# Performance work log

Measured on AMD Instinct MI355X. Metric: run time of the kernel, lower is better.

The kernel has to match this reference:

```python
import jax, jax.numpy as jnp
import numpy as np

B, A, C, G = 16, 65472, 81, 50
POS_THRESH = 0.5        # positive_threshold
NEG_POS_RATIO = 3
CENTER_VAR, SIZE_VAR = 0.1, 0.2   # standard SSD encoding variances
BETA = 1.0 / 9


def _make_boxes(key, shape):
    # random valid corner-form boxes in [0,1]
    k1, k2 = jax.random.split(key)
    cxy = jax.random.uniform(k1, shape + (2,), minval=0.1, maxval=0.9)
    wh = jax.random.uniform(k2, shape + (2,), minval=0.05, maxval=0.3)
    lo = jnp.clip(cxy - wh / 2, 0.0, 1.0)
    hi = jnp.clip(cxy + wh / 2, 0.0, 1.0)
    return jnp.concatenate([lo, hi], axis=-1).astype(jnp.float32)


def setup_inputs() -> dict:
    key = jax.random.key(0)
    ks = jax.random.split(key, 6)
    confidence = jax.random.normal(ks[0], (B, A, C), dtype=jnp.float32)
    predicted_locations = jax.random.normal(ks[1], (B, A, 4), dtype=jnp.float32)
    boxes = _make_boxes(ks[2], (B, G))
    labels = jax.random.randint(ks[3], (B, G, 1), 1, C).astype(jnp.float32)
    gts = jnp.concatenate([boxes, labels], axis=-1)          # (B, G, 5)
    counts = jax.random.randint(ks[4], (B,), 1, G + 1)       # valid gt per image
    anchors = _make_boxes(ks[5], (A,))                        # corner form
    return {"confidence": confidence, "predicted_locations": predicted_locations,
            "gts": gts, "counts": counts, "anchors": anchors}


def _center_form(b):
    # corner (x1,y1,x2,y2) -> center (cx,cy,w,h)
    return jnp.concatenate([(b[..., :2] + b[..., 2:]) * 0.5,
                            b[..., 2:] - b[..., :2]], axis=-1)


def _iou(a, b):
    # a: (A,4), b: (G,4), corner form -> (A,G)
    lt = jnp.maximum(a[:, None, :2], b[None, :, :2])
    rb = jnp.minimum(a[:, None, 2:], b[None, :, 2:])
    wh = jnp.clip(rb - lt, 0.0)
    inter = wh[..., 0] * wh[..., 1]
    area_a = (a[:, 2] - a[:, 0]) * (a[:, 3] - a[:, 1])
    area_b = (b[:, 2] - b[:, 0]) * (b[:, 3] - b[:, 1])
    return inter / (area_a[:, None] + area_b[None, :] - inter + 1e-10)


def _encode(matched, anchors_c):
    m = _center_form(matched)
    g_cxcy = (m[..., :2] - anchors_c[..., :2]) / (anchors_c[..., 2:] * CENTER_VAR)
    g_wh = jnp.log(m[..., 2:] / anchors_c[..., 2:] + 1e-10) / SIZE_VAR
    return jnp.concatenate([g_cxcy, g_wh], axis=-1)


def _match(gt, count, anchors, anchors_c):
    # gt: (G,5), count: scalar int
    boxes = gt[:, :4]
    glabels = gt[:, 4].astype(jnp.int32)
    valid = jnp.arange(boxes.shape[0]) < count
    ious = jnp.where(valid[None, :], _iou(anchors, boxes), -1.0)  # (A,G)
    best_iou = ious.max(axis=1)          # best gt per anchor
    best_idx = ious.argmax(axis=1)
    best_anchor = ious.argmax(axis=0)    # best anchor per gt (G,)
    # force-match: each valid gt claims its best anchor (invalid -> dropped)
    scat = jnp.where(valid, best_anchor, anchors.shape[0])
    best_idx = best_idx.at[scat].set(jnp.arange(boxes.shape[0]), mode='drop')
    best_iou = best_iou.at[scat].set(2.0, mode='drop')
    labels = jnp.where(best_iou < POS_THRESH, 0, glabels[best_idx])  # (A,)
    loc = _encode(boxes[best_idx], anchors_c)                         # (A,4)
    return labels, loc


def reference(confidence, predicted_locations, gts, counts, anchors):
    anchors_c = _center_form(anchors)
    labels, gt_locations = jax.vmap(
        lambda g, c: _match(g, c, anchors, anchors_c))(gts, counts)
    labels = jax.lax.stop_gradient(labels)
    gt_locations = jax.lax.stop_gradient(gt_locations)

    logp = jax.nn.log_softmax(confidence, axis=2)          # (B,A,C)
    pos_mask = labels > 0
    num_pos_b = pos_mask.sum(axis=1)                        # (B,)

    # hard negative mining on background loss (positives excluded via -inf)
    mining = jnp.where(pos_mask, -jnp.inf, jax.lax.stop_gradient(-logp[:, :, 0]))
    order = jnp.argsort(-mining, axis=1)   # descending
    rank = jnp.argsort(order, axis=1)
    neg_mask = rank < (NEG_POS_RATIO * num_pos_b)[:, None]
    mask = pos_mask | neg_mask

    num_pos = jnp.maximum(1.0, pos_mask.sum().astype(jnp.float32))

    # masked cross-entropy (sum) == F.cross_entropy(conf[mask], labels[mask], 'sum')
    ce = -jnp.take_along_axis(logp, labels[..., None], axis=2)[..., 0]
    classification_loss = jnp.sum(jnp.where(mask, ce, 0.0)) / (num_pos * 4.0)

    # smooth L1 over positive anchors only
    n = jnp.abs(predicted_locations - gt_locations)
    sl1 = jnp.where(n < BETA, 0.5 * n * n / BETA, n - 0.5 * BETA)
    localisation_loss = jnp.sum(jnp.where(pos_mask[..., None], sl1, 0.0)) / (num_pos * 4.0)
    return (localisation_loss, classification_loss)
```

## Files before the change

### kernel.cpp

```cpp
#include <hip/hip_runtime.h>
#include <math.h>

#define Bn 16
#define An 65472
#define Cn 81
#define Gn 50
#define ROWS 64
#define NCH 8
#define CHUNK_F4 1296
#define LD_T 216
#define LD_K 6
#define NCHH 4
#define NBUCK 1024
#define LISTCAP 8192

static_assert((Bn * (long long)An) % (ROWS * NCH) == 0, "grid covers rows exactly");
static_assert(LD_T * LD_K == CHUNK_F4, "uniform load split");
static_assert((An / 4) % NCHH == 0, "hist chunks divide");

constexpr float POS_THRESH_C = 0.5f;
constexpr float BETA_C = 1.0f / 9.0f;

typedef const __attribute__((address_space(1))) void GPTR;
typedef __attribute__((address_space(3))) void LPTR;

__global__ __launch_bounds__(256) void k1a(const float* __restrict__ anchors,
                                           const float* __restrict__ gts,
                                           const int* __restrict__ counts,
                                           float* __restrict__ best_iou,
                                           int* __restrict__ best_idx,
                                           int* __restrict__ numpos_b,
                                           float* __restrict__ fsums) {
    const int b = blockIdx.y;
    __shared__ float sg[Gn * 5];
    const int t = threadIdx.x;
    if (blockIdx.x == 0 && b == 0) {
        if (t < Bn) numpos_b[t] = 0;
        if (t == Bn) { fsums[0] = 0.f; fsums[1] = 0.f; }
    }
    if (t < Gn * 5) sg[t] = gts[b * Gn * 5 + t];
    __syncthreads();
    const int a = blockIdx.x * 256 + t;
    if (a >= An) return;
    const int cnt = counts[b];
    const float4 av = ((const float4*)anchors)[a];
    const float area_a = (av.z - av.x) * (av.w - av.y);
    float best = -1.0f;
    int bidx = 0;
    for (int g = 0; g < Gn; ++g) {
        if (g >= cnt) break;
        const float bx0 = sg[g * 5 + 0], by0 = sg[g * 5 + 1];
        const float bx1 = sg[g * 5 + 2], by1 = sg[g * 5 + 3];
        const float w = fmaxf(fminf(av.z, bx1) - fmaxf(av.x, bx0), 0.f);
        const float h = fmaxf(fminf(av.w, by1) - fmaxf(av.y, by0), 0.f);
        const float inter = w * h;
        const float area_b = (bx1 - bx0) * (by1 - by0);
        const float iou = inter / (area_a + area_b - inter + 1e-10f);
        if (iou > best) { best = iou; bidx = g; }
    }
    best_iou[(size_t)b * An + a] = best;
    best_idx[(size_t)b * An + a] = bidx;
}

__global__ __launch_bounds__(256) void k1b(const float* __restrict__ anchors,
                                           const float* __restrict__ gts,
                                           const int* __restrict__ counts,
                                           int* __restrict__ best_anchor) {
    const int b = blockIdx.y, g = blockIdx.x;
    const int t = threadIdx.x;
    const int cnt = counts[b];
    if (g >= cnt) { if (t == 0) best_anchor[b * Gn + g] = 0; return; }
    const float bx0 = gts[(b * Gn + g) * 5 + 0], by0 = gts[(b * Gn + g) * 5 + 1];
    const float bx1 = gts[(b * Gn + g) * 5 + 2], by1 = gts[(b * Gn + g) * 5 + 3];
    const float area_b = (bx1 - bx0) * (by1 - by0);
    const float4* a4 = (const float4*)anchors;
    float best = -2.f;
    int bidx = 0x7fffffff;
    for (int base = t; base < An; base += 1024) {
        const int a1 = base + 256, a2 = base + 512, a3 = base + 768;
        const float4 av0 = a4[base];
        float4 av1, av2, av3;
        const bool ok1 = a1 < An, ok2 = a2 < An, ok3 = a3 < An;
        if (ok1) av1 = a4[a1];
        if (ok2) av2 = a4[a2];
        if (ok3) av3 = a4[a3];
        {
            const float area_a = (av0.z - av0.x) * (av0.w - av0.y);
            const float w = fmaxf(fminf(av0.z, bx1) - fmaxf(av0.x, bx0), 0.f);
            const float h = fmaxf(fminf(av0.w, by1) - fmaxf(av0.y, by0), 0.f);
            const float inter = w * h;
            const float iou = inter / (area_a + area_b - inter + 1e-10f);
            if (iou > best) { best = iou; bidx = base; }
        }
        if (ok1) {
            const float area_a = (av1.z - av1.x) * (av1.w - av1.y);
            const float w = fmaxf(fminf(av1.z, bx1) - fmaxf(av1.x, bx0), 0.f);
            const float h = fmaxf(fminf(av1.w, by1) - fmaxf(av1.y, by0), 0.f);
            const float inter = w * h;
            const float iou = inter / (area_a + area_b - inter + 1e-10f);
            if (iou > best) { best = iou; bidx = a1; }
        }
        if (ok2) {
            const float area_a = (av2.z - av2.x) * (av2.w - av2.y);
            const float w = fmaxf(fminf(av2.z, bx1) - fmaxf(av2.x, bx0), 0.f);
            const float h = fmaxf(fminf(av2.w, by1) - fmaxf(av2.y, by0), 0.f);
            const float inter = w * h;
            const float iou = inter / (area_a + area_b - inter + 1e-10f);
            if (iou > best) { best = iou; bidx = a2; }
        }
        if (ok3) {
            const float area_a = (av3.z - av3.x) * (av3.w - av3.y);
            const float w = fmaxf(fminf(av3.z, bx1) - fmaxf(av3.x, bx0), 0.f);
            const float h = fmaxf(fminf(av3.w, by1) - fmaxf(av3.y, by0), 0.f);
            const float inter = w * h;
            const float iou = inter / (area_a + area_b - inter + 1e-10f);
            if (iou > best) { best = iou; bidx = a3; }
        }
    }
    __shared__ float rv[256];
    __shared__ int ri[256];
    rv[t] = best; ri[t] = bidx;
    __syncthreads();
    for (int s = 128; s > 0; s >>= 1) {
        if (t < s) {
            const float fv = rv[t + s]; const int fi = ri[t + s];
            if (fv > rv[t] || (fv == rv[t] && fi < ri[t])) { rv[t] = fv; ri[t] = fi; }
        }
        __syncthreads();
    }
    if (t == 0) best_anchor[b * Gn + g] = ri[0];
}

__global__ __launch_bounds__(64) void k1c(const int* __restrict__ counts,
                                          const int* __restrict__ best_anchor,
                                          float* __restrict__ best_iou,
                                          int* __restrict__ best_idx) {
    const int b = threadIdx.x;
    if (b >= Bn) return;
    const int cnt = counts[b] < Gn ? counts[b] : Gn;
    for (int g = 0; g < cnt; ++g) {
        const int a = best_anchor[b * Gn + g];
        best_idx[(size_t)b * An + a] = g;
        best_iou[(size_t)b * An + a] = 2.0f;
    }
}

__global__ __launch_bounds__(256) void k2(const float* __restrict__ conf,
                                          const float* __restrict__ pred,
                                          const float* __restrict__ gts,
                                          const float* __restrict__ anchors,
                                          const float* __restrict__ best_iou,
                                          const int* __restrict__ best_idx,
                                          int* __restrict__ v_int,
                                          int* __restrict__ numpos_b,
                                          float* __restrict__ fsums) {
    __shared__ __align__(16) float sc[2][ROWS * Cn];
    __shared__ float s_ce[4], s_loc[4];
    __shared__ int s_n0[4], s_n1[4];
    const int t = threadIdx.x;
    const size_t rowbase = (size_t)blockIdx.x * (ROWS * NCH);
    const float* gbase = conf + rowbase * Cn;

    if (t < LD_T) {
#pragma unroll
        for (int k = 0; k < LD_K; ++k) {
            const int c = k * LD_T + t;
            __builtin_amdgcn_global_load_lds((GPTR*)(gbase + c * 4), (LPTR*)(&sc[0][0] + c * 4), 16, 0, 0);
        }
    }

    const int bf = (int)(rowbase / An);
    const int r = t >> 2, h = t & 3;
    const int j0 = h * 20 + (h != 0);
    const int j1 = 21 + h * 20;
    float ce = 0.f, loc = 0.f;
    int n0 = 0, n1 = 0;

    for (int cc = 0; cc < NCH; ++cc) {
        if (cc + 1 < NCH) {
            if (t < LD_T) {
                const float* gp = gbase + (size_t)(cc + 1) * (ROWS * Cn);
                float* lp = &sc[(cc + 1) & 1][0];
#pragma unroll
                for (int k = 0; k < LD_K; ++k) {
                    const int c = k * LD_T + t;
                    __builtin_amdgcn_global_load_lds((GPTR*)(gp + c * 4), (LPTR*)(lp + c * 4), 16, 0, 0);
                }
            }
            asm volatile("s_waitcnt vmcnt(6)" ::: "memory");
        } else {
            asm volatile("s_waitcnt vmcnt(0)" ::: "memory");
        }
        __builtin_amdgcn_sched_barrier(0);
        __builtin_amdgcn_s_barrier();
        asm volatile("" ::: "memory");

        const float* row = &sc[cc & 1][0] + r * Cn;
        float s0 = 0.f, s1 = 0.f;
        for (int j = j0; j + 1 < j1; j += 2) { s0 += __expf(row[j]); s1 += __expf(row[j + 1]); }
        if (((j1 - j0) & 1) != 0) s0 += __expf(row[j1 - 1]);
        float s = s0 + s1;
        s += __shfl_xor(s, 1);
        s += __shfl_xor(s, 2);
        const float lse = logf(s);

        if (h == 0) {
            const size_t gidx = rowbase + (size_t)cc * ROWS + r;
            const int b = (int)(gidx / An);
            const int a = (int)(gidx - (size_t)b * An);
            const float bi = best_iou[gidx];
            const int idx = best_idx[gidx];
            if (bi < POS_THRESH_C) {
                v_int[gidx] = __float_as_int(lse - row[0]);
            } else {
                v_int[gidx] = -1;
                int lab = (int)gts[((size_t)b * Gn + idx) * 5 + 4];
                lab = lab < 0 ? 0 : (lab > Cn - 1 ? Cn - 1 : lab);
                ce += lse - row[lab];
                if (b == bf) ++n0; else ++n1;
                const float bx0 = gts[((size_t)b * Gn + idx) * 5 + 0];
                const float by0 = gts[((size_t)b * Gn + idx) * 5 + 1];
                const float bx1 = gts[((size_t)b * Gn + idx) * 5 + 2];
                const float by1 = gts[((size_t)b * Gn + idx) * 5 + 3];
                const float4 av = ((const float4*)anchors)[a];
                const float acx = (av.x + av.z) * 0.5f, acy = (av.y + av.w) * 0.5f;
                const float aw = av.z - av.x, ah = av.w - av.y;
                float tt[4];
                tt[0] = ((bx0 + bx1) * 0.5f - acx) / (aw * 0.1f);
                tt[1] = ((by0 + by1) * 0.5f - acy) / (ah * 0.1f);
                tt[2] = logf((bx1 - bx0) / aw + 1e-10f) / 0.2f;
                tt[3] = logf((by1 - by0) / ah + 1e-10f) / 0.2f;
                const float4 p = ((const float4*)pred)[gidx];
                const float pk[4] = {p.x, p.y, p.z, p.w};
#pragma unroll
                for (int k = 0; k < 4; ++k) {
                    const float nn = fabsf(pk[k] - tt[k]);
                    loc += (nn < BETA_C) ? 0.5f * nn * nn / BETA_C : nn - 0.5f * BETA_C;
                }
            }
        }
        asm volatile("" ::: "memory");
        __builtin_amdgcn_s_barrier();
    }

#pragma unroll
    for (int off = 32; off > 0; off >>= 1) {
        ce += __shfl_down(ce, off);
        loc += __shfl_down(loc, off);
        n0 += __shfl_down(n0, off);
        n1 += __shfl_down(n1, off);
    }
    if ((t & 63) == 0) {
        const int w = t >> 6;
        s_ce[w] = ce; s_loc[w] = loc; s_n0[w] = n0; s_n1[w] = n1;
    }
    __syncthreads();
    if (t == 0) {
        const float CE = s_ce[0] + s_ce[1] + s_ce[2] + s_ce[3];
        const float LC = s_loc[0] + s_loc[1] + s_loc[2] + s_loc[3];
        const int N0 = s_n0[0] + s_n0[1] + s_n0[2] + s_n0[3];
        const int N1 = s_n1[0] + s_n1[1] + s_n1[2] + s_n1[3];
        if (CE != 0.f) atomicAdd(&fsums[0], CE);
        if (LC != 0.f) atomicAdd(&fsums[1], LC);
        if (N0 > 0) atomicAdd(&numpos_b[bf], N0);
        if (N1 > 0) atomicAdd(&numpos_b[bf + 1], N1);
    }
}

__global__ __launch_bounds__(256) void k3a(const int* __restrict__ v_int,
                                           int* __restrict__ ghist) {
    const int b = blockIdx.y, c = blockIdx.x;
    __shared__ int lh[NBUCK];
    const int t = threadIdx.x;
    for (int i = t; i < NBUCK; i += 256) lh[i] = 0;
    __syncthreads();
    const int CH4 = (An / 4) / NCHH;
    const int4* v4 = (const int4*)(v_int + (size_t)b * An) + c * CH4;
    for (int i = t; i < CH4; i += 256) {
        const int4 x4 = v4[i];
        const int xs[4] = {x4.x, x4.y, x4.z, x4.w};
#pragma unroll
        for (int q = 0; q < 4; ++q) {
            const int x = xs[q];
            if (x < 0) continue;
            int bin = (int)(__int_as_float(x) * 64.0f);
            bin = bin > NBUCK - 1 ? NBUCK - 1 : bin;
            atomicAdd(&lh[bin], 1);
        }
    }
    __syncthreads();
    for (int i = t; i < NBUCK; i += 256)
        ghist[((size_t)(b * NCHH + c)) * NBUCK + i] = lh[i];
}

__global__ __launch_bounds__(256) void k3b(const int* __restrict__ v_int,
                                           const int* __restrict__ ghist,
                                           const int* __restrict__ numpos_b,
                                           float* __restrict__ neg_sum_b) {
    const int b = blockIdx.x, t = threadIdx.x;
    const int npb = numpos_b[b];
    const long long K = 3LL * npb;
    const int n_nonpos = An - npb;
    __shared__ int h[NBUCK];
    __shared__ int gsfx[256];
    __shared__ int s_kt, s_r, s_m;
    __shared__ float fred[256];
    __shared__ float list[LISTCAP];
    if (K <= 0) { if (t == 0) neg_sum_b[b] = 0.f; return; }
    const int4* v4 = (const int4*)(v_int + (size_t)b * An);
    const int N4 = An / 4;
    const bool selAll = (K >= n_nonpos);
    int kt = -1, r = 0;
    if (!selAll) {
        const int* gh = ghist + (size_t)(b * NCHH) * NBUCK;
        for (int i = t; i < NBUCK; i += 256) {
            int v = 0;
#pragma unroll
            for (int c = 0; c < NCHH; ++c) v += gh[c * NBUCK + i];
            h[i] = v;
        }
        if (t == 0) s_m = 0;
        __syncthreads();
        gsfx[t] = h[4 * t] + h[4 * t + 1] + h[4 * t + 2] + h[4 * t + 3];
        __syncthreads();
        if (t == 0) {
            int acc = 0;
            for (int i = 255; i >= 0; --i) { const int tmp = gsfx[i]; gsfx[i] = acc; acc += tmp; }
        }
        __syncthreads();
        {
            const int base = 4 * t;
            int cg[4];
            cg[3] = gsfx[t];
            cg[2] = cg[3] + h[base + 3];
            cg[1] = cg[2] + h[base + 2];
            cg[0] = cg[1] + h[base + 1];
#pragma unroll
            for (int q = 0; q < 4; ++q) {
                if (cg[q] < K && K <= cg[q] + (long long)h[base + q]) {
                    s_kt = base + q; s_r = (int)(K - cg[q]);
                }
            }
        }
        __syncthreads();
        kt = s_kt; r = s_r;
    } else {
        if (t == 0) s_m = 0;
        __syncthreads();
    }
    float s = 0.f;
    for (int i = t; i < N4; i += 256) {
        const int4 x4 = v4[i];
        const int xs[4] = {x4.x, x4.y, x4.z, x4.w};
#pragma unroll
        for (int q = 0; q < 4; ++q) {
            const int x = xs[q];
            if (x < 0) continue;
            const float v = __int_as_float(x);
            if (selAll) { s += v; continue; }
            int bin = (int)(v * 64.0f);
            bin = bin > NBUCK - 1 ? NBUCK - 1 : bin;
            if (bin > kt) s += v;
            else if (bin == kt) {
                const int p = atomicAdd(&s_m, 1);
                if (p < LISTCAP) list[p] = v;
            }
        }
    }
    __syncthreads();
    if (!selAll) {
        int M = s_m; M = M > LISTCAP ? LISTCAP : M;
        for (int i = t; i < M; i += 256) {
            const float x = list[i];
            int cnt = 0;
            for (int j = 0; j < M; ++j) {
                const float y = list[j];
                cnt += (y > x) || (y == x && j < i);
            }
            if (cnt < r) s += x;
        }
    }
    fred[t] = s;
    __syncthreads();
    for (int st = 128; st > 0; st >>= 1) {
        if (t < st) fred[t] += fred[t + st];
        __syncthreads();
    }
    if (t == 0) neg_sum_b[b] = fred[0];
}

__global__ __launch_bounds__(64) void k4(const int* __restrict__ numpos_b,
                                         const float* __restrict__ fsums,
                                         const float* __restrict__ neg_sum_b,
                                         float* __restrict__ out) {
    if (threadIdx.x == 0) {
        int np = 0;
        for (int b = 0; b < Bn; ++b) np += numpos_b[b];
        const float num_pos = fmaxf(1.f, (float)np);
        const float denom = num_pos * 4.f;
        float neg = 0.f;
        for (int b = 0; b < Bn; ++b) neg += neg_sum_b[b];
        out[0] = fsums[1] / denom;
        out[1] = (fsums[0] + neg) / denom;
    }
}

extern "C" void kernel_launch(void* const* d_in, const int* in_sizes, int n_in,
                              void* d_out, int out_size, void* d_ws, size_t ws_size,
                              hipStream_t stream) {
    const float* conf    = (const float*)d_in[0];
    const float* pred    = (const float*)d_in[1];
    const float* gts     = (const float*)d_in[2];
    const int*   counts  = (const int*)d_in[3];
    const float* anchors = (const float*)d_in[4];
    float* out = (float*)d_out;

    const size_t BA = (size_t)Bn * An;
    char* w = (char*)d_ws;
    float* best_iou    = (float*)w; w += BA * sizeof(float);
    int*   best_idx    = (int*)w;   w += BA * sizeof(int);
    int*   v_int       = (int*)w;   w += BA * sizeof(int);
    int*   best_anchor = (int*)w;   w += Bn * Gn * sizeof(int);
    int*   numpos_b    = (int*)w;   w += 64;
    float* fsums       = (float*)w; w += 64;
    float* neg_sum_b   = (float*)w; w += 64;
    int*   ghist       = (int*)best_iou;

    hipLaunchKernelGGL(k1a, dim3((An + 255) / 256, Bn), dim3(256), 0, stream,
                       anchors, gts, counts, best_iou, best_idx, numpos_b, fsums);
    hipLaunchKernelGGL(k1b, dim3(Gn, Bn), dim3(256), 0, stream,
                       anchors, gts, counts, best_anchor);
    hipLaunchKernelGGL(k1c, dim3(1), dim3(64), 0, stream,
                       counts, best_anchor, best_iou, best_idx);
    hipLaunchKernelGGL(k2, dim3((unsigned)(BA / (ROWS * NCH))), dim3(256), 0, stream,
                       conf, pred, gts, anchors, best_iou, best_idx,
                       v_int, numpos_b, fsums);
    hipLaunchKernelGGL(k3a, dim3(NCHH, Bn), dim3(256), 0, stream, v_int, ghist);
    hipLaunchKernelGGL(k3b, dim3(Bn), dim3(256), 0, stream,
                       v_int, ghist, numpos_b, neg_sum_b);
    hipLaunchKernelGGL(k4, dim3(1), dim3(64), 0, stream, numpos_b, fsums, neg_sum_b, out);
}
```

Measured before the change: 668.0 us.

## Fuse anchor matching into loss kernel and merge histogram and finalize stages

The per-anchor best-IoU matching moves into the main confidence kernel. Four lanes per row split the ground-truth boxes and reduce with shuffles, and each block applies the forced best-anchor overrides from shared memory. This removes the best_iou/best_idx buffers, their global round trip, and the k1a/k1c launches. The histogram kernel is folded into the selection kernel, which now reads the data twice with only 16 blocks. The final reduction runs as a last-block-done atomic, dropping two more launches at the cost of extra IoU work inside the memory-bound kernel.

```diff
diff --git a/kernel.cpp b/kernel.cpp
--- a/kernel.cpp
+++ b/kernel.cpp
@@ -7,67 +7,37 @@
 #define Gn 50
 #define ROWS 64
 #define NCH 8
+#define BROWS (ROWS * NCH)
 #define CHUNK_F4 1296
 #define LD_T 216
 #define LD_K 6
-#define NCHH 4
 #define NBUCK 1024
 #define LISTCAP 8192
 
-static_assert((Bn * (long long)An) % (ROWS * NCH) == 0, "grid covers rows exactly");
+static_assert((Bn * (long long)An) % BROWS == 0, "grid covers rows exactly");
 static_assert(LD_T * LD_K == CHUNK_F4, "uniform load split");
-static_assert((An / 4) % NCHH == 0, "hist chunks divide");
 
 constexpr float POS_THRESH_C = 0.5f;
 constexpr float BETA_C = 1.0f / 9.0f;
 
 typedef const __attribute__((address_space(1))) void GPTR;
 typedef __attribute__((address_space(3))) void LPTR;
-
-__global__ __launch_bounds__(256) void k1a(const float* __restrict__ anchors,
-                                           const float* __restrict__ gts,
-                                           const int* __restrict__ counts,
-                                           float* __restrict__ best_iou,
-                                           int* __restrict__ best_idx,
-                                           int* __restrict__ numpos_b,
-                                           float* __restrict__ fsums) {
-    const int b = blockIdx.y;
-    __shared__ float sg[Gn * 5];
-    const int t = threadIdx.x;
-    if (blockIdx.x == 0 && b == 0) {
-        if (t < Bn) numpos_b[t] = 0;
-        if (t == Bn) { fsums[0] = 0.f; fsums[1] = 0.f; }
-    }
-    if (t < Gn * 5) sg[t] = gts[b * Gn * 5 + t];
-    __syncthreads();
-    const int a = blockIdx.x * 256 + t;
-    if (a >= An) return;
-    const int cnt = counts[b];
-    const float4 av = ((const float4*)anchors)[a];
-    const float area_a = (av.z - av.x) * (av.w - av.y);
-    float best = -1.0f;
-    int bidx = 0;
-    for (int g = 0; g < Gn; ++g) {
-        if (g >= cnt) break;
-        const float bx0 = sg[g * 5 + 0], by0 = sg[g * 5 + 1];
-        const float bx1 = sg[g * 5 + 2], by1 = sg[g * 5 + 3];
-        const float w = fmaxf(fminf(av.z, bx1) - fmaxf(av.x, bx0), 0.f);
-        const float h = fmaxf(fminf(av.w, by1) - fmaxf(av.y, by0), 0.f);
-        const float inter = w * h;
-        const float area_b = (bx1 - bx0) * (by1 - by0);
-        const float iou = inter / (area_a + area_b - inter + 1e-10f);
-        if (iou > best) { best = iou; bidx = g; }
-    }
-    best_iou[(size_t)b * An + a] = best;
-    best_idx[(size_t)b * An + a] = bidx;
-}
 
 __global__ __launch_bounds__(256) void k1b(const float* __restrict__ anchors,
                                            const float* __restrict__ gts,
                                            const int* __restrict__ counts,
-                                           int* __restrict__ best_anchor) {
+                                           int* __restrict__ best_anchor,
+                                           int* __restrict__ numpos_b,
+                                           float* __restrict__ fsums,
+                                           float* __restrict__ neg_sum_b,
+                                           int* __restrict__ done) {
     const int b = blockIdx.y, g = blockIdx.x;
     const int t = threadIdx.x;
+    if (g == 0 && b == 0) {
+        if (t < Bn) { numpos_b[t] = 0; neg_sum_b[t] = 0.f; }
+        if (t == Bn) { fsums[0] = 0.f; fsums[1] = 0.f; }
+        if (t == Bn + 1) *done = 0;
+    }
     const int cnt = counts[b];
     if (g >= cnt) { if (t == 0) best_anchor[b * Gn + g] = 0; return; }
     const float bx0 = gts[(b * Gn + g) * 5 + 0], by0 = gts[(b * Gn + g) * 5 + 1];
@@ -131,35 +101,50 @@
     if (t == 0) best_anchor[b * Gn + g] = ri[0];
 }
 
-__global__ __launch_bounds__(64) void k1c(const int* __restrict__ counts,
-                                          const int* __restrict__ best_anchor,
-                                          float* __restrict__ best_iou,
-                                          int* __restrict__ best_idx) {
-    const int b = threadIdx.x;
-    if (b >= Bn) return;
-    const int cnt = counts[b] < Gn ? counts[b] : Gn;
-    for (int g = 0; g < cnt; ++g) {
-        const int a = best_anchor[b * Gn + g];
-        best_idx[(size_t)b * An + a] = g;
-        best_iou[(size_t)b * An + a] = 2.0f;
-    }
-}
-
 __global__ __launch_bounds__(256) void k2(const float* __restrict__ conf,
                                           const float* __restrict__ pred,
                                           const float* __restrict__ gts,
+                                          const int* __restrict__ counts,
                                           const float* __restrict__ anchors,
-                                          const float* __restrict__ best_iou,
-                                          const int* __restrict__ best_idx,
+                                          const int* __restrict__ best_anchor,
                                           int* __restrict__ v_int,
                                           int* __restrict__ numpos_b,
                                           float* __restrict__ fsums) {
     __shared__ __align__(16) float sc[2][ROWS * Cn];
+    __shared__ float4 sb[2][Gn];
+    __shared__ int    sba[2][Gn];
+    __shared__ int    scnt[2];
+    __shared__ short  ov_g[BROWS];
     __shared__ float s_ce[4], s_loc[4];
     __shared__ int s_n0[4], s_n1[4];
     const int t = threadIdx.x;
-    const size_t rowbase = (size_t)blockIdx.x * (ROWS * NCH);
+    const size_t rowbase = (size_t)blockIdx.x * BROWS;
     const float* gbase = conf + rowbase * Cn;
+    const int bf = (int)(rowbase / An);
+    const size_t split = (size_t)(bf + 1) * An;
+
+    ov_g[t] = -1; ov_g[t + 256] = -1;
+    if (t < 2) scnt[t] = (bf + t < Bn) ? counts[bf + t] : 0;
+    if (t < 2 * Gn) {
+        const int bi = t / Gn, g = t - bi * Gn;
+        if (bf + bi < Bn) {
+            const float* gp = &gts[((size_t)(bf + bi) * Gn + g) * 5];
+            sb[bi][g] = make_float4(gp[0], gp[1], gp[2], gp[3]);
+            sba[bi][g] = best_anchor[(bf + bi) * Gn + g];
+        }
+    }
+    __syncthreads();
+    if (t == 0) {
+        for (int bi = 0; bi < 2; ++bi) {
+            if (bf + bi >= Bn) break;
+            const int cnt = scnt[bi];
+            for (int g = 0; g < cnt; ++g) {
+                const int lr = (int)((size_t)(bf + bi) * An + sba[bi][g] - rowbase);
+                if (lr >= 0 && lr < BROWS) ov_g[lr] = (short)g;
+            }
+        }
+    }
+    __syncthreads();
 
     if (t < LD_T) {
 #pragma unroll
@@ -169,7 +154,6 @@
         }
     }
 
-    const int bf = (int)(rowbase / An);
     const int r = t >> 2, h = t & 3;
     const int j0 = h * 20 + (h != 0);
     const int j1 = 21 + h * 20;
@@ -204,32 +188,51 @@
         s += __shfl_xor(s, 2);
         const float lse = logf(s);
 
+        const int lrow = cc * ROWS + r;
+        const size_t gidx = rowbase + lrow;
+        const int b = (gidx >= split) ? bf + 1 : bf;
+        const int bi2 = b - bf;
+        const int a = (int)(gidx - (size_t)b * An);
+        const float4 av = ((const float4*)anchors)[a];
+        const float area_a = (av.z - av.x) * (av.w - av.y);
+        const int cnt = scnt[bi2];
+        float bestv = -1.0f;
+        int bidx = 0x7fffffff;
+        for (int g = h; g < cnt; g += 4) {
+            const float4 bb = sb[bi2][g];
+            const float w = fmaxf(fminf(av.z, bb.z) - fmaxf(av.x, bb.x), 0.f);
+            const float hh = fmaxf(fminf(av.w, bb.w) - fmaxf(av.y, bb.y), 0.f);
+            const float inter = w * hh;
+            const float area_b = (bb.z - bb.x) * (bb.w - bb.y);
+            const float iou = inter / (area_a + area_b - inter + 1e-10f);
+            if (iou > bestv) { bestv = iou; bidx = g; }
+        }
+        {
+            float fv = __shfl_xor(bestv, 1); int fi = __shfl_xor(bidx, 1);
+            if (fv > bestv || (fv == bestv && fi < bidx)) { bestv = fv; bidx = fi; }
+            fv = __shfl_xor(bestv, 2); fi = __shfl_xor(bidx, 2);
+            if (fv > bestv || (fv == bestv && fi < bidx)) { bestv = fv; bidx = fi; }
+        }
+
         if (h == 0) {
-            const size_t gidx = rowbase + (size_t)cc * ROWS + r;
-            const int b = (int)(gidx / An);
-            const int a = (int)(gidx - (size_t)b * An);
-            const float bi = best_iou[gidx];
-            const int idx = best_idx[gidx];
-            if (bi < POS_THRESH_C) {
+            const int og = ov_g[lrow];
+            if (og >= 0) { bidx = og; bestv = 2.0f; }
+            if (bestv < POS_THRESH_C) {
                 v_int[gidx] = __float_as_int(lse - row[0]);
             } else {
                 v_int[gidx] = -1;
-                int lab = (int)gts[((size_t)b * Gn + idx) * 5 + 4];
+                int lab = (int)gts[((size_t)b * Gn + bidx) * 5 + 4];
                 lab = lab < 0 ? 0 : (lab > Cn - 1 ? Cn - 1 : lab);
                 ce += lse - row[lab];
                 if (b == bf) ++n0; else ++n1;
-                const float bx0 = gts[((size_t)b * Gn + idx) * 5 + 0];
-                const float by0 = gts[((size_t)b * Gn + idx) * 5 + 1];
-                const float bx1 = gts[((size_t)b * Gn + idx) * 5 + 2];
-                const float by1 = gts[((size_t)b * Gn + idx) * 5 + 3];
-                const float4 av = ((const float4*)anchors)[a];
+                const float4 bb = sb[bi2][bidx];
                 const float acx = (av.x + av.z) * 0.5f, acy = (av.y + av.w) * 0.5f;
                 const float aw = av.z - av.x, ah = av.w - av.y;
                 float tt[4];
-                tt[0] = ((bx0 + bx1) * 0.5f - acx) / (aw * 0.1f);
-                tt[1] = ((by0 + by1) * 0.5f - acy) / (ah * 0.1f);
-                tt[2] = logf((bx1 - bx0) / aw + 1e-10f) / 0.2f;
-                tt[3] = logf((by1 - by0) / ah + 1e-10f) / 0.2f;
+                tt[0] = ((bb.x + bb.z) * 0.5f - acx) / (aw * 0.1f);
+                tt[1] = ((bb.y + bb.w) * 0.5f - acy) / (ah * 0.1f);
+                tt[2] = logf((bb.z - bb.x) / aw + 1e-10f) / 0.2f;
+                tt[3] = logf((bb.w - bb.y) / ah + 1e-10f) / 0.2f;
                 const float4 p = ((const float4*)pred)[gidx];
                 const float pk[4] = {p.x, p.y, p.z, p.w};
 #pragma unroll
@@ -267,36 +270,12 @@
     }
 }
 
-__global__ __launch_bounds__(256) void k3a(const int* __restrict__ v_int,
-                                           int* __restrict__ ghist) {
-    const int b = blockIdx.y, c = blockIdx.x;
-    __shared__ int lh[NBUCK];
-    const int t = threadIdx.x;
-    for (int i = t; i < NBUCK; i += 256) lh[i] = 0;
-    __syncthreads();
-    const int CH4 = (An / 4) / NCHH;
-    const int4* v4 = (const int4*)(v_int + (size_t)b * An) + c * CH4;
-    for (int i = t; i < CH4; i += 256) {
-        const int4 x4 = v4[i];
-        const int xs[4] = {x4.x, x4.y, x4.z, x4.w};
-#pragma unroll
-        for (int q = 0; q < 4; ++q) {
-            const int x = xs[q];
-            if (x < 0) continue;
-            int bin = (int)(__int_as_float(x) * 64.0f);
-            bin = bin > NBUCK - 1 ? NBUCK - 1 : bin;
-            atomicAdd(&lh[bin], 1);
-        }
-    }
-    __syncthreads();
-    for (int i = t; i < NBUCK; i += 256)
-        ghist[((size_t)(b * NCHH + c)) * NBUCK + i] = lh[i];
-}
-
 __global__ __launch_bounds__(256) void k3b(const int* __restrict__ v_int,
-                                           const int* __restrict__ ghist,
                                            const int* __restrict__ numpos_b,
-                                           float* __restrict__ neg_sum_b) {
+                                           const float* __restrict__ fsums,
+                                           float* __restrict__ neg_sum_b,
+                                           int* __restrict__ done,
+                                           float* __restrict__ out) {
     const int b = blockIdx.x, t = threadIdx.x;
     const int npb = numpos_b[b];
     const long long K = 3LL * npb;
@@ -306,102 +285,111 @@
     __shared__ int s_kt, s_r, s_m;
     __shared__ float fred[256];
     __shared__ float list[LISTCAP];
-    if (K <= 0) { if (t == 0) neg_sum_b[b] = 0.f; return; }
     const int4* v4 = (const int4*)(v_int + (size_t)b * An);
     const int N4 = An / 4;
     const bool selAll = (K >= n_nonpos);
-    int kt = -1, r = 0;
-    if (!selAll) {
-        const int* gh = ghist + (size_t)(b * NCHH) * NBUCK;
-        for (int i = t; i < NBUCK; i += 256) {
-            int v = 0;
-#pragma unroll
-            for (int c = 0; c < NCHH; ++c) v += gh[c * NBUCK + i];
-            h[i] = v;
-        }
-        if (t == 0) s_m = 0;
+    float blocksum = 0.f;
+    if (K > 0) {
+        int kt = -1, r = 0;
+        if (!selAll) {
+            for (int i = t; i < NBUCK; i += 256) h[i] = 0;
+            if (t == 0) s_m = 0;
+            __syncthreads();
+            for (int i = t; i < N4; i += 256) {
+                const int4 x4 = v4[i];
+                const int xs[4] = {x4.x, x4.y, x4.z, x4.w};
+#pragma unroll
+                for (int q = 0; q < 4; ++q) {
+                    const int x = xs[q];
+                    if (x < 0) continue;
+                    int bin = (int)(__int_as_float(x) * 64.0f);
+                    bin = bin > NBUCK - 1 ? NBUCK - 1 : bin;
+                    atomicAdd(&h[bin], 1);
+                }
+            }
+            __syncthreads();
+            gsfx[t] = h[4 * t] + h[4 * t + 1] + h[4 * t + 2] + h[4 * t + 3];
+            __syncthreads();
+            if (t == 0) {
+                int acc = 0;
+                for (int i = 255; i >= 0; --i) { const int tmp = gsfx[i]; gsfx[i] = acc; acc += tmp; }
+            }
+            __syncthreads();
+            {
+                const int base = 4 * t;
+                int cg[4];
+                cg[3] = gsfx[t];
+                cg[2] = cg[3] + h[base + 3];
+                cg[1] = cg[2] + h[base + 2];
+                cg[0] = cg[1] + h[base + 1];
+#pragma unroll
+                for (int q = 0; q < 4; ++q) {
+                    if (cg[q] < K && K <= cg[q] + (long long)h[base + q]) {
+                        s_kt = base + q; s_r = (int)(K - cg[q]);
+                    }
+                }
+            }
+            __syncthreads();
+            kt = s_kt; r = s_r;
+        } else {
+            if (t == 0) s_m = 0;
+            __syncthreads();
+        }
+        float s = 0.f;
+        for (int i = t; i < N4; i += 256) {
+            const int4 x4 = v4[i];
+            const int xs[4] = {x4.x, x4.y, x4.z, x4.w};
+#pragma unroll
+            for (int q = 0; q < 4; ++q) {
+                const int x = xs[q];
+                if (x < 0) continue;
+                const float v = __int_as_float(x);
+                if (selAll) { s += v; continue; }
+                int bin = (int)(v * 64.0f);
+                bin = bin > NBUCK - 1 ? NBUCK - 1 : bin;
+                if (bin > kt) s += v;
+                else if (bin == kt) {
+                    const int p = atomicAdd(&s_m, 1);
+                    if (p < LISTCAP) list[p] = v;
+                }
+            }
+        }
         __syncthreads();
-        gsfx[t] = h[4 * t] + h[4 * t + 1] + h[4 * t + 2] + h[4 * t + 3];
+        if (!selAll) {
+            int M = s_m; M = M > LISTCAP ? LISTCAP : M;
+            for (int i = t; i < M; i += 256) {
+                const float x = list[i];
+                int cnt = 0;
+                for (int j = 0; j < M; ++j) {
+                    const float y = list[j];
+                    cnt += (y > x) || (y == x && j < i);
+                }
+                if (cnt < r) s += x;
+            }
+        }
+        fred[t] = s;
         __syncthreads();
-        if (t == 0) {
-            int acc = 0;
-            for (int i = 255; i >= 0; --i) { const int tmp = gsfx[i]; gsfx[i] = acc; acc += tmp; }
-        }
-        __syncthreads();
-        {
-            const int base = 4 * t;
-            int cg[4];
-            cg[3] = gsfx[t];
-            cg[2] = cg[3] + h[base + 3];
-            cg[1] = cg[2] + h[base + 2];
-            cg[0] = cg[1] + h[base + 1];
-#pragma unroll
-            for (int q = 0; q < 4; ++q) {
-                if (cg[q] < K && K <= cg[q] + (long long)h[base + q]) {
-                    s_kt = base + q; s_r = (int)(K - cg[q]);
-                }
-            }
-        }
-        __syncthreads();
-        kt = s_kt; r = s_r;
-    } else {
-        if (t == 0) s_m = 0;
-        __syncthreads();
-    }
-    float s = 0.f;
-    for (int i = t; i < N4; i += 256) {
-        const int4 x4 = v4[i];
-        const int xs[4] = {x4.x, x4.y, x4.z, x4.w};
-#pragma unroll
-        for (int q = 0; q < 4; ++q) {
-            const int x = xs[q];
-            if (x < 0) continue;
-            const float v = __int_as_float(x);
-            if (selAll) { s += v; continue; }
-            int bin = (int)(v * 64.0f);
-            bin = bin > NBUCK - 1 ? NBUCK - 1 : bin;
-            if (bin > kt) s += v;
-            else if (bin == kt) {
-                const int p = atomicAdd(&s_m, 1);
-                if (p < LISTCAP) list[p] = v;
-            }
-        }
-    }
-    __syncthreads();
-    if (!selAll) {
-        int M = s_m; M = M > LISTCAP ? LISTCAP : M;
-        for (int i = t; i < M; i += 256) {
-            const float x = list[i];
-            int cnt = 0;
-            for (int j = 0; j < M; ++j) {
-                const float y = list[j];
-                cnt += (y > x) || (y == x && j < i);
-            }
-            if (cnt < r) s += x;
-        }
-    }
-    fred[t] = s;
-    __syncthreads();
-    for (int st = 128; st > 0; st >>= 1) {
-        if (t < st) fred[t] += fred[t + st];
-        __syncthreads();
-    }
-    if (t == 0) neg_sum_b[b] = fred[0];
-}
-
-__global__ __launch_bounds__(64) void k4(const int* __restrict__ numpos_b,
-                                         const float* __restrict__ fsums,
-                                         const float* __restrict__ neg_sum_b,
-                                         float* __restrict__ out) {
-    if (threadIdx.x == 0) {
-        int np = 0;
-        for (int b = 0; b < Bn; ++b) np += numpos_b[b];
-        const float num_pos = fmaxf(1.f, (float)np);
-        const float denom = num_pos * 4.f;
-        float neg = 0.f;
-        for (int b = 0; b < Bn; ++b) neg += neg_sum_b[b];
-        out[0] = fsums[1] / denom;
-        out[1] = (fsums[0] + neg) / denom;
+        for (int st = 128; st > 0; st >>= 1) {
+            if (t < st) fred[t] += fred[t + st];
+            __syncthreads();
+        }
+        blocksum = fred[0];
+    }
+    if (t == 0) {
+        atomicExch(&neg_sum_b[b], blocksum);
+        __threadfence();
+        const int old = atomicAdd(done, 1);
+        if (old == Bn - 1) {
+            float neg = 0.f;
+            for (int bb = 0; bb < Bn; ++bb)
+                neg += atomicAdd(&neg_sum_b[bb], 0.0f);
+            int np = 0;
+            for (int bb = 0; bb < Bn; ++bb) np += numpos_b[bb];
+            const float num_pos = fmaxf(1.f, (float)np);
+            const float denom = num_pos * 4.f;
+            out[0] = fsums[1] / denom;
+            out[1] = (fsums[0] + neg) / denom;
+        }
     }
 }
 
@@ -417,26 +405,19 @@
 
     const size_t BA = (size_t)Bn * An;
     char* w = (char*)d_ws;
-    float* best_iou    = (float*)w; w += BA * sizeof(float);
-    int*   best_idx    = (int*)w;   w += BA * sizeof(int);
     int*   v_int       = (int*)w;   w += BA * sizeof(int);
     int*   best_anchor = (int*)w;   w += Bn * Gn * sizeof(int);
     int*   numpos_b    = (int*)w;   w += 64;
     float* fsums       = (float*)w; w += 64;
     float* neg_sum_b   = (float*)w; w += 64;
-    int*   ghist       = (int*)best_iou;
-
-    hipLaunchKernelGGL(k1a, dim3((An + 255) / 256, Bn), dim3(256), 0, stream,
-                       anchors, gts, counts, best_iou, best_idx, numpos_b, fsums);
+    int*   done        = (int*)w;   w += 64;
+
     hipLaunchKernelGGL(k1b, dim3(Gn, Bn), dim3(256), 0, stream,
-                       anchors, gts, counts, best_anchor);
-    hipLaunchKernelGGL(k1c, dim3(1), dim3(64), 0, stream,
-                       counts, best_anchor, best_iou, best_idx);
-    hipLaunchKernelGGL(k2, dim3((unsigned)(BA / (ROWS * NCH))), dim3(256), 0, stream,
-                       conf, pred, gts, anchors, best_iou, best_idx,
+                       anchors, gts, counts, best_anchor,
+                       numpos_b, fsums, neg_sum_b, done);
+    hipLaunchKernelGGL(k2, dim3((unsigned)(BA / BROWS)), dim3(256), 0, stream,
+                       conf, pred, gts, counts, anchors, best_anchor,
                        v_int, numpos_b, fsums);
-    hipLaunchKernelGGL(k3a, dim3(NCHH, Bn), dim3(256), 0, stream, v_int, ghist);
     hipLaunchKernelGGL(k3b, dim3(Bn), dim3(256), 0, stream,
-                       v_int, ghist, numpos_b, neg_sum_b);
-    hipLaunchKernelGGL(k4, dim3(1), dim3(64), 0, stream, numpos_b, fsums, neg_sum_b, out);
+                       v_int, numpos_b, fsums, neg_sum_b, done, out);
 }
```

Result: no change. 671.2 us (+0.5%).
